# Optimization experiments

Hardware: AMD Instinct MI355X
Metric: run time of the kernel (lower is better)

## Reference

```python
import jax, jax.numpy as jnp
import numpy as np

D_MODEL = 1024
NUM_HEADS = 16


def setup_inputs() -> dict:
    key = jax.random.key(0)
    ks = jax.random.split(key, 5)
    B, S, D = 4, 2048, D_MODEL
    # std=1.0 trunc_normal in original init; plain normal is fine for a numeric reference,
    # but scale down to keep logits numerically sane under fp32.
    x = jax.random.normal(ks[0], (B, S, D), dtype=jnp.float32)
    wq = jax.random.normal(ks[1], (D, D), dtype=jnp.float32) * 0.02
    wk = jax.random.normal(ks[2], (D, D), dtype=jnp.float32) * 0.02
    wv = jax.random.normal(ks[3], (D, D), dtype=jnp.float32) * 0.02
    wo = jax.random.normal(ks[4], (D, D), dtype=jnp.float32) * 0.02
    return {"x": x, "q_proj_weight": wq, "k_proj_weight": wk,
            "v_proj_weight": wv, "o_proj_weight": wo}


def reference(x, q_proj_weight, k_proj_weight, v_proj_weight, o_proj_weight):
    B, S, D = x.shape
    H = NUM_HEADS
    dh = D // H
    # unfused QKV projections (weights applied as x @ W.T, matching torch)
    q = jnp.einsum('bsd,ed->bse', x, q_proj_weight).reshape(B, S, H, dh).transpose(0, 2, 1, 3)
    k = jnp.einsum('bsd,ed->bse', x, k_proj_weight).reshape(B, S, H, dh).transpose(0, 2, 1, 3)
    v = jnp.einsum('bsd,ed->bse', x, v_proj_weight).reshape(B, S, H, dh).transpose(0, 2, 1, 3)
    scale = 1.0 / jnp.sqrt(jnp.asarray(dh, dtype=x.dtype))
    scores = jnp.einsum('bhqd,bhkd->bhqk', q, k) * scale  # [B,H,S,S]
    causal = jnp.tril(jnp.ones((S, S), dtype=bool))       # True = keep
    scores = jnp.where(causal[None, None], scores, -jnp.inf)
    attn = jax.nn.softmax(scores, axis=-1)
    out = jnp.einsum('bhqk,bhkd->bhqd', attn, v)           # [B,H,S,dh]
    out = out.transpose(0, 2, 1, 3).reshape(B, S, D)
    return jnp.einsum('bsd,ed->bse', out, o_proj_weight)
```

## Files before the change

### kernel.cpp

```cpp
#include <hip/hip_runtime.h>
#include <hip/hip_bf16.h>
#include <stdint.h>


#define S_LEN 2048
#define DM 1024
#define NH 16
#define NB 4
#define DH 64
#define BS (NB * S_LEN)
#define SM_SHIFT 16.0f

typedef __attribute__((ext_vector_type(4))) float f32x4;
typedef __attribute__((ext_vector_type(16))) float f32x16;
typedef __attribute__((ext_vector_type(8))) short bf16x8;
typedef __attribute__((ext_vector_type(4))) short s16x4;

static __device__ __forceinline__ float bf2f(short u) {
    union { float f; uint32_t i; } c; c.i = ((uint32_t)(uint16_t)u) << 16; return c.f;
}
static __device__ __forceinline__ short f2bf(float f) {
    union { float f; uint32_t i; } c; c.f = f;
    uint32_t r = (c.i + 0x7FFFu + ((c.i >> 16) & 1u)) >> 16;
    return (short)r;
}

__global__ void cast_kernel(const float* __restrict__ in, short* __restrict__ out, int n4) {
    int i = blockIdx.x * blockDim.x + threadIdx.x;
    if (i >= n4) return;
    f32x4 v = *(const f32x4*)(in + (size_t)i * 4);
    s16x4 o;
    o[0] = f2bf(v[0]); o[1] = f2bf(v[1]); o[2] = f2bf(v[2]); o[3] = f2bf(v[3]);
    *(s16x4*)(out + (size_t)i * 4) = o;
}

__global__ void cast4_kernel(const float* __restrict__ a, const float* __restrict__ b,
                             const float* __restrict__ c, const float* __restrict__ d,
                             short* __restrict__ out, int n4per) {
    int z = blockIdx.y;
    const float* in = z == 0 ? a : z == 1 ? b : z == 2 ? c : d;
    int i = blockIdx.x * blockDim.x + threadIdx.x;
    if (i >= n4per) return;
    f32x4 v = *(const f32x4*)(in + (size_t)i * 4);
    s16x4 o;
    o[0] = f2bf(v[0]); o[1] = f2bf(v[1]); o[2] = f2bf(v[2]); o[3] = f2bf(v[3]);
    *(s16x4*)(out + (size_t)z * n4per * 4 + (size_t)i * 4) = o;
}

template <int MODE>
__global__ __launch_bounds__(256) void gemm_bt(const short* __restrict__ A,
                                               const short* __restrict__ Bm,
                                               void* __restrict__ Cout,
                                               int M, int N, int Kd) {
    __shared__ __align__(16) short lA[2][128 * 32];
    __shared__ __align__(16) short lB[2][128 * 32];
    const int tid = threadIdx.x;
    const int lane = tid & 63;
    const int wave = tid >> 6;
    const int mb = blockIdx.x;
    const int nb = blockIdx.y;
    const int wm = (wave >> 1) * 64;
    const int wn = (wave & 1) * 64;
    const int c16 = lane & 15;
    const int g = lane >> 4;

    auto stage = [&](int buf, int kb) {
        for (int i = 0; i < 2; i++) {
            int row = i * 64 + wave * 16 + (lane >> 2);
            int col = (lane & 3) * 8;
            const short* srcA = A + (size_t)(mb * 128 + row) * Kd + kb * 32 + col;
            const short* srcB = Bm + (size_t)(nb * 128 + row) * Kd + kb * 32 + col;
            __builtin_amdgcn_global_load_lds(
                (const __attribute__((address_space(1))) void*)srcA,
                (__attribute__((address_space(3))) void*)(&lA[buf][i * 2048 + wave * 512]),
                16, 0, 0);
            __builtin_amdgcn_global_load_lds(
                (const __attribute__((address_space(1))) void*)srcB,
                (__attribute__((address_space(3))) void*)(&lB[buf][i * 2048 + wave * 512]),
                16, 0, 0);
        }
    };

    f32x4 acc[4][4];
    f32x4 zero = {0.f, 0.f, 0.f, 0.f};
    for (int i = 0; i < 4; i++)
        for (int j = 0; j < 4; j++) acc[i][j] = zero;

    const int nk = Kd >> 5;
    stage(0, 0);
    __syncthreads();
    for (int t = 0; t < nk; t++) {
        int cur = t & 1;
        if (t + 1 < nk) stage(cur ^ 1, t + 1);
        bf16x8 af[4], bfr[4];
        for (int i = 0; i < 4; i++) {
            af[i]  = *(const bf16x8*)&lA[cur][(wm + i * 16 + c16) * 32 + g * 8];
            bfr[i] = *(const bf16x8*)&lB[cur][(wn + i * 16 + c16) * 32 + g * 8];
        }
        for (int mi = 0; mi < 4; mi++)
            for (int ni = 0; ni < 4; ni++)
                acc[mi][ni] = __builtin_amdgcn_mfma_f32_16x16x32_bf16(af[mi], bfr[ni], acc[mi][ni], 0, 0, 0);
        __syncthreads();
    }

    for (int mi = 0; mi < 4; mi++) {
        int row0 = mb * 128 + wm + mi * 16 + g * 4;
        for (int ni = 0; ni < 4; ni++) {
            int col = nb * 128 + wn + ni * 16 + c16;
            f32x4 a = acc[mi][ni];
            for (int r = 0; r < 4; r++) {
                int rr = row0 + r;
                if (MODE == 0) {
                    ((float*)Cout)[(size_t)rr * N + col] = a[r];
                } else if (MODE == 1) {
                    ((short*)Cout)[(size_t)rr * N + col] = f2bf(a[r]);
                } else {
                    int b = rr >> 11, s = rr & 2047, h = col >> 6, d = col & 63;
                    int kl = s & 31;
                    int pos = kl ^ ((((kl >> 2) ^ (kl >> 3)) & 1) ? 12 : 0);
                    ((short*)Cout)[(((size_t)(b * NH + h) * 64 + (s >> 5)) * 64 + d) * 32 + pos] = f2bf(a[r]);
                }
            }
        }
    }
}

__global__ __launch_bounds__(256, 4) void attn_stg_kernel(const short* __restrict__ Q,
                                                          const short* __restrict__ K,
                                                          const short* __restrict__ Vt,
                                                          short* __restrict__ Oo) {
    __shared__ __align__(16) char stg[4][8192];
    __shared__ float lL[4][32];
    const int lane = threadIdx.x & 63;
    const int wave = threadIdx.x >> 6;
    const int j = blockIdx.x >> 6;
    const int bh = blockIdx.x & 63;
    const int b = bh >> 4, h = bh & 15;
    const int l31 = lane & 31;
    const int hi = lane >> 5;
    const bool three = (j <= 20);

    const int qtA = 63 - j, qtB = j;
    const int nkA = qtA + 1, nkB = qtB + 1;
    int qt, t0, t1;
    if (three) {
        if (wave < 3) { qt = qtA; t0 = (nkA * wave) / 3; t1 = (nkA * (wave + 1)) / 3; }
        else          { qt = qtB; t0 = 0; t1 = nkB; }
    } else {
        int half = wave & 1;
        if (wave < 2) { int hh = (nkA + 1) >> 1; qt = qtA; t0 = half ? hh : 0; t1 = half ? nkA : hh; }
        else          { int hh = (nkB + 1) >> 1; qt = qtB; t0 = half ? hh : 0; t1 = half ? nkB : hh; }
    }
    const int q0 = qt * 32;
    const int qrow = q0 + l31;

    const short* Qb = Q + (size_t)b * S_LEN * DM + h * DH;
    const short* Kb = K + (size_t)b * S_LEN * DM + h * DH;
    const short* Vb = Vt + (size_t)bh * S_LEN * DH;
    const float QSCALE = 0.125f * 1.4426950408889634f;

    char* wbK = stg[wave];
    char* wbV = stg[wave] + 4096;

    bf16x8 qf[4];
    #pragma unroll
    for (int c = 0; c < 4; c++) {
        bf16x8 t = *(const bf16x8*)(Qb + (size_t)qrow * DM + c * 16 + hi * 8);
        #pragma unroll
        for (int jj = 0; jj < 8; jj++) t[jj] = f2bf(bf2f(t[jj]) * QSCALE);
        qf[c] = t;
    }

    f32x16 o0, o1;
    #pragma unroll
    for (int r = 0; r < 16; r++) { o0[r] = 0.f; o1[r] = 0.f; }
    float l_r = 0.f;

    const int i_ = lane;
    const int kcol = (((i_ & 7) ^ (i_ >> 3)) << 3);
    const int krow = (i_ >> 3);
    const int vcol = (((i_ & 3) ^ ((i_ >> 2) & 3)) << 3);
    const int vrow = (i_ >> 2);
    auto stage = [&](int kb) {
        const short* ks = Kb + (size_t)(kb * 32 + krow) * DM + kcol;
        #pragma unroll
        for (int c = 0; c < 4; c++)
            __builtin_amdgcn_global_load_lds(
                (const __attribute__((address_space(1))) void*)(ks + (size_t)c * 8 * DM),
                (__attribute__((address_space(3))) void*)(wbK + c * 1024), 16, 0, 0);
        const short* vs = Vb + (size_t)kb * 2048 + (size_t)vrow * 32 + vcol;
        #pragma unroll
        for (int c = 0; c < 4; c++)
            __builtin_amdgcn_global_load_lds(
                (const __attribute__((address_space(1))) void*)(vs + (size_t)c * 16 * 32),
                (__attribute__((address_space(3))) void*)(wbV + c * 1024), 16, 0, 0);
    };

    bf16x8 kf[4], vf[4];
    const int kx = (l31 & 7) << 4;
    const int vx = (l31 & 3) << 4;
    auto readfrags = [&]() {
        #pragma unroll
        for (int cc = 0; cc < 4; cc++)
            kf[cc] = *(const bf16x8*)(wbK + l31 * 128 + ((cc * 32 + hi * 16) ^ kx));
        vf[0] = *(const bf16x8*)(wbV + l31 * 64 + ((hi * 16) ^ vx));
        vf[1] = *(const bf16x8*)(wbV + l31 * 64 + ((32 + hi * 16) ^ vx));
        vf[2] = *(const bf16x8*)(wbV + (32 + l31) * 64 + ((hi * 16) ^ vx));
        vf[3] = *(const bf16x8*)(wbV + (32 + l31) * 64 + ((32 + hi * 16) ^ vx));
    };

    if (t0 < t1) {
        stage(t0);
        asm volatile("s_waitcnt vmcnt(0)" ::: "memory");
        __builtin_amdgcn_sched_barrier(0);
        readfrags();
    }

    for (int kb = t0; kb < t1; kb++) {
        const int kbase = kb * 32;
        f32x16 st;
        #pragma unroll
        for (int r = 0; r < 16; r++) st[r] = 0.f;
        __builtin_amdgcn_s_setprio(1);
        st = __builtin_amdgcn_mfma_f32_32x32x16_bf16(kf[0], qf[0], st, 0, 0, 0);
        st = __builtin_amdgcn_mfma_f32_32x32x16_bf16(kf[1], qf[1], st, 0, 0, 0);
        st = __builtin_amdgcn_mfma_f32_32x32x16_bf16(kf[2], qf[2], st, 0, 0, 0);
        st = __builtin_amdgcn_mfma_f32_32x32x16_bf16(kf[3], qf[3], st, 0, 0, 0);
        __builtin_amdgcn_s_setprio(0);

        if (kb + 1 < t1) {
            asm volatile("s_waitcnt lgkmcnt(0)" ::: "memory");
            __builtin_amdgcn_sched_barrier(0);
            stage(kb + 1);
        }

        float p[16];
        if (kb == qt) {
            #pragma unroll
            for (int r = 0; r < 16; r++) {
                int kl = (r & 3) + 8 * (r >> 2) + 4 * hi;
                float v = (kbase + kl > qrow) ? -1e30f : st[r];
                p[r] = exp2f(v - SM_SHIFT);
            }
        } else {
            #pragma unroll
            for (int r = 0; r < 16; r++) p[r] = exp2f(st[r] - SM_SHIFT);
        }

        float s01 = (p[0] + p[1]) + (p[2] + p[3]);
        float s23 = (p[4] + p[5]) + (p[6] + p[7]);
        float s45 = (p[8] + p[9]) + (p[10] + p[11]);
        float s67 = (p[12] + p[13]) + (p[14] + p[15]);
        l_r += (s01 + s23) + (s45 + s67);

        union { uint32_t u[4]; bf16x8 v; } c0, c1;
        #pragma unroll
        for (int i = 0; i < 4; i++) {
            union { float f; uint32_t u; } a0, a1, b0, b1;
            a0.f = p[2 * i];     a1.f = p[2 * i + 1];
            b0.f = p[8 + 2 * i]; b1.f = p[8 + 2 * i + 1];
            c0.u[i] = __builtin_amdgcn_perm(a1.u + 0x8000u, a0.u + 0x8000u, 0x07060302u);
            c1.u[i] = __builtin_amdgcn_perm(b1.u + 0x8000u, b0.u + 0x8000u, 0x07060302u);
        }

        __builtin_amdgcn_s_setprio(1);
        o0 = __builtin_amdgcn_mfma_f32_32x32x16_bf16(vf[0], c0.v, o0, 0, 0, 0);
        o0 = __builtin_amdgcn_mfma_f32_32x32x16_bf16(vf[1], c1.v, o0, 0, 0, 0);
        o1 = __builtin_amdgcn_mfma_f32_32x32x16_bf16(vf[2], c0.v, o1, 0, 0, 0);
        o1 = __builtin_amdgcn_mfma_f32_32x32x16_bf16(vf[3], c1.v, o1, 0, 0, 0);
        __builtin_amdgcn_s_setprio(0);

        if (kb + 1 < t1) {
            asm volatile("s_waitcnt vmcnt(0)" ::: "memory");
            __builtin_amdgcn_sched_barrier(0);
            readfrags();
        }
    }

    l_r += __shfl_xor(l_r, 32);

    const bool publisher = three ? (wave == 1 || wave == 2) : (wave == 1 || wave == 3);
    if (publisher) {
        short* pb = (short*)stg[wave];
        #pragma unroll
        for (int dc = 0; dc < 2; dc++)
            #pragma unroll
            for (int g2 = 0; g2 < 4; g2++) {
                int d = dc * 32 + g2 * 8 + hi * 4;
                s16x4 v4;
                #pragma unroll
                for (int rr = 0; rr < 4; rr++) v4[rr] = f2bf((dc ? o1 : o0)[g2 * 4 + rr]);
                *(s16x4*)(pb + l31 * 68 + d) = v4;
            }
        if (!hi) lL[wave][l31] = l_r;
    }
    if (three && wave == 3) {
        float inv = 1.0f / l_r;
        size_t base = ((size_t)b * S_LEN + qrow) * DM + h * DH;
        #pragma unroll
        for (int dc = 0; dc < 2; dc++)
            #pragma unroll
            for (int g2 = 0; g2 < 4; g2++) {
                s16x4 ov;
                #pragma unroll
                for (int rr = 0; rr < 4; rr++)
                    ov[rr] = f2bf((dc ? o1 : o0)[g2 * 4 + rr] * inv);
                *(s16x4*)(Oo + base + dc * 32 + g2 * 8 + hi * 4) = ov;
            }
    }
    __syncthreads();

    const bool merger = three ? (wave == 0) : (wave == 0 || wave == 2);
    if (merger) {
        const short* p1 = (const short*)stg[wave + 1];
        float L = l_r + lL[wave + 1][l31];
        const short* p2 = nullptr;
        if (three) { p2 = (const short*)stg[2]; L += lL[2][l31]; }
        float inv = 1.0f / L;
        size_t base = ((size_t)b * S_LEN + qrow) * DM + h * DH;
        #pragma unroll
        for (int dc = 0; dc < 2; dc++)
            #pragma unroll
            for (int g2 = 0; g2 < 4; g2++) {
                int d = dc * 32 + g2 * 8 + hi * 4;
                s16x4 a = *(const s16x4*)(p1 + l31 * 68 + d);
                s16x4 ov;
                #pragma unroll
                for (int rr = 0; rr < 4; rr++) {
                    float acc = (dc ? o1 : o0)[g2 * 4 + rr] + bf2f(a[rr]);
                    if (three) acc += bf2f(p2[l31 * 68 + d + rr]);
                    ov[rr] = f2bf(acc * inv);
                }
                *(s16x4*)(Oo + base + d) = ov;
            }
    }
}

extern "C" void kernel_launch(void* const* d_in, const int* in_sizes, int n_in,
                              void* d_out, int out_size, void* d_ws, size_t ws_size,
                              hipStream_t stream) {
    const float* x  = (const float*)d_in[0];
    const float* wq = (const float*)d_in[1];
    const float* wk = (const float*)d_in[2];
    const float* wv = (const float*)d_in[3];
    const float* wo = (const float*)d_in[4];
    float* out = (float*)d_out;

    short* ws = (short*)d_ws;
    size_t off = 0;
    short* xb  = ws + off; off += (size_t)BS * DM;
    short* wqb = ws + off; off += (size_t)DM * DM;
    short* wkb = ws + off; off += (size_t)DM * DM;
    short* wvb = ws + off; off += (size_t)DM * DM;
    short* wob = ws + off; off += (size_t)DM * DM;
    short* Qb  = ws + off; off += (size_t)BS * DM;
    short* Kb  = ws + off; off += (size_t)BS * DM;
    short* Vtb = ws + off; off += (size_t)BS * DM;
    short* attn_o = xb;

    {
        int n4 = (BS * DM) / 4;
        cast_kernel<<<n4 / 256, 256, 0, stream>>>(x, xb, n4);
        int w4 = (DM * DM) / 4;
        cast4_kernel<<<dim3(w4 / 256, 4), 256, 0, stream>>>(wq, wk, wv, wo, wqb, w4);
    }

    dim3 pgrid(BS / 128, DM / 128);
    gemm_bt<1><<<pgrid, 256, 0, stream>>>(xb, wqb, Qb,  BS, DM, DM);
    gemm_bt<1><<<pgrid, 256, 0, stream>>>(xb, wkb, Kb,  BS, DM, DM);
    gemm_bt<2><<<pgrid, 256, 0, stream>>>(xb, wvb, Vtb, BS, DM, DM);

    attn_stg_kernel<<<dim3(2048), 256, 0, stream>>>(Qb, Kb, Vtb, attn_o);

    gemm_bt<0><<<pgrid, 256, 0, stream>>>(attn_o, wob, out, BS, DM, DM);
}
```

Before: 206.3 us.

## Double-buffer K/V fragments in registers and prefetch two tiles ahead

```diff
diff --git a/kernel.cpp b/kernel.cpp
--- a/kernel.cpp
+++ b/kernel.cpp
@@ -125,10 +125,10 @@
     }
 }
 
-__global__ __launch_bounds__(256, 4) void attn_stg_kernel(const short* __restrict__ Q,
-                                                          const short* __restrict__ K,
-                                                          const short* __restrict__ Vt,
-                                                          short* __restrict__ Oo) {
+__global__ __launch_bounds__(256) void attn_stg_kernel(const short* __restrict__ Q,
+                                                       const short* __restrict__ K,
+                                                       const short* __restrict__ Vt,
+                                                       short* __restrict__ Oo) {
     __shared__ __align__(16) char stg[4][8192];
     __shared__ float lL[4][32];
     const int lane = threadIdx.x & 63;
@@ -196,10 +196,9 @@
                 (__attribute__((address_space(3))) void*)(wbV + c * 1024), 16, 0, 0);
     };
 
-    bf16x8 kf[4], vf[4];
     const int kx = (l31 & 7) << 4;
     const int vx = (l31 & 3) << 4;
-    auto readfrags = [&]() {
+    auto readfrags = [&](bf16x8 (&kf)[4], bf16x8 (&vf)[4]) {
         #pragma unroll
         for (int cc = 0; cc < 4; cc++)
             kf[cc] = *(const bf16x8*)(wbK + l31 * 128 + ((cc * 32 + hi * 16) ^ kx));
@@ -209,33 +208,29 @@
         vf[3] = *(const bf16x8*)(wbV + (32 + l31) * 64 + ((32 + hi * 16) ^ vx));
     };
 
-    if (t0 < t1) {
-        stage(t0);
-        asm volatile("s_waitcnt vmcnt(0)" ::: "memory");
-        __builtin_amdgcn_sched_barrier(0);
-        readfrags();
-    }
-
-    for (int kb = t0; kb < t1; kb++) {
-        const int kbase = kb * 32;
+    bf16x8 kfA[4], vfA[4], kfB[4], vfB[4];
+
+    auto tile = [&](int t, bf16x8 (&kfC)[4], bf16x8 (&vfC)[4],
+                    bf16x8 (&kfN)[4], bf16x8 (&vfN)[4]) {
+        const int kbase = t * 32;
         f32x16 st;
         #pragma unroll
         for (int r = 0; r < 16; r++) st[r] = 0.f;
         __builtin_amdgcn_s_setprio(1);
-        st = __builtin_amdgcn_mfma_f32_32x32x16_bf16(kf[0], qf[0], st, 0, 0, 0);
-        st = __builtin_amdgcn_mfma_f32_32x32x16_bf16(kf[1], qf[1], st, 0, 0, 0);
-        st = __builtin_amdgcn_mfma_f32_32x32x16_bf16(kf[2], qf[2], st, 0, 0, 0);
-        st = __builtin_amdgcn_mfma_f32_32x32x16_bf16(kf[3], qf[3], st, 0, 0, 0);
+        st = __builtin_amdgcn_mfma_f32_32x32x16_bf16(kfC[0], qf[0], st, 0, 0, 0);
+        st = __builtin_amdgcn_mfma_f32_32x32x16_bf16(kfC[1], qf[1], st, 0, 0, 0);
+        st = __builtin_amdgcn_mfma_f32_32x32x16_bf16(kfC[2], qf[2], st, 0, 0, 0);
+        st = __builtin_amdgcn_mfma_f32_32x32x16_bf16(kfC[3], qf[3], st, 0, 0, 0);
         __builtin_amdgcn_s_setprio(0);
 
-        if (kb + 1 < t1) {
-            asm volatile("s_waitcnt lgkmcnt(0)" ::: "memory");
+        if (t + 1 < t1) {
+            asm volatile("s_waitcnt vmcnt(0)" ::: "memory");
             __builtin_amdgcn_sched_barrier(0);
-            stage(kb + 1);
+            readfrags(kfN, vfN);
         }
 
         float p[16];
-        if (kb == qt) {
+        if (t == qt) {
             #pragma unroll
             for (int r = 0; r < 16; r++) {
                 int kl = (r & 3) + 8 * (r >> 2) + 4 * hi;
@@ -246,7 +241,6 @@
             #pragma unroll
             for (int r = 0; r < 16; r++) p[r] = exp2f(st[r] - SM_SHIFT);
         }
-
         float s01 = (p[0] + p[1]) + (p[2] + p[3]);
         float s23 = (p[4] + p[5]) + (p[6] + p[7]);
         float s45 = (p[8] + p[9]) + (p[10] + p[11]);
@@ -263,19 +257,34 @@
             c1.u[i] = __builtin_amdgcn_perm(b1.u + 0x8000u, b0.u + 0x8000u, 0x07060302u);
         }
 
+        if (t + 2 < t1) {
+            asm volatile("s_waitcnt lgkmcnt(0)" ::: "memory");
+            __builtin_amdgcn_sched_barrier(0);
+            stage(t + 2);
+        }
+
         __builtin_amdgcn_s_setprio(1);
-        o0 = __builtin_amdgcn_mfma_f32_32x32x16_bf16(vf[0], c0.v, o0, 0, 0, 0);
-        o0 = __builtin_amdgcn_mfma_f32_32x32x16_bf16(vf[1], c1.v, o0, 0, 0, 0);
-        o1 = __builtin_amdgcn_mfma_f32_32x32x16_bf16(vf[2], c0.v, o1, 0, 0, 0);
-        o1 = __builtin_amdgcn_mfma_f32_32x32x16_bf16(vf[3], c1.v, o1, 0, 0, 0);
+        o0 = __builtin_amdgcn_mfma_f32_32x32x16_bf16(vfC[0], c0.v, o0, 0, 0, 0);
+        o0 = __builtin_amdgcn_mfma_f32_32x32x16_bf16(vfC[1], c1.v, o0, 0, 0, 0);
+        o1 = __builtin_amdgcn_mfma_f32_32x32x16_bf16(vfC[2], c0.v, o1, 0, 0, 0);
+        o1 = __builtin_amdgcn_mfma_f32_32x32x16_bf16(vfC[3], c1.v, o1, 0, 0, 0);
         __builtin_amdgcn_s_setprio(0);
-
-        if (kb + 1 < t1) {
-            asm volatile("s_waitcnt vmcnt(0)" ::: "memory");
-            __builtin_amdgcn_sched_barrier(0);
-            readfrags();
-        }
-    }
+    };
+
+    {
+        stage(t0);
+        asm volatile("s_waitcnt vmcnt(0)" ::: "memory");
+        __builtin_amdgcn_sched_barrier(0);
+        readfrags(kfA, vfA);
+        if (t0 + 1 < t1) stage(t0 + 1);
+    }
+    int t = t0;
+    while (t + 1 < t1) {
+        tile(t,     kfA, vfA, kfB, vfB);
+        tile(t + 1, kfB, vfB, kfA, vfA);
+        t += 2;
+    }
+    if (t < t1) tile(t, kfA, vfA, kfB, vfB);
 
     l_r += __shfl_xor(l_r, 32);
 
```

After: 218.0 us. 5.7% more time.
